# Optimization experiments

Hardware: AMD Instinct MI355X
Metric: run time of the kernel (lower is better)

Reference implementation:

```python
import jax, jax.numpy as jnp
import numpy as np

N = 100000
E = 1600000
EMB3 = 192   # embedding_size * 3
F_LAT = 64   # latency_feature_size
F_OUT = 128  # latency_feature_size * 2 (GATConv out_feats, 1 head)
NEG_SLOPE = 0.2  # DGL GATConv default leaky_relu slope


def setup_inputs() -> dict:
    key = jax.random.key(0)
    ks = jax.random.split(key, 9)
    return {
        "embed": jax.random.normal(ks[0], (N, EMB3), dtype=jnp.float32),
        "src": jax.random.randint(ks[1], (E,), 0, N, dtype=jnp.int64)
               if jax.config.jax_enable_x64 else jax.random.randint(ks[1], (E,), 0, N, dtype=jnp.int32),
        "dst": jax.random.randint(ks[2], (E,), 0, N, dtype=jnp.int32),
        "W_lin": jax.random.normal(ks[3], (EMB3, F_LAT), dtype=jnp.float32) * 0.05,
        "b_lin": jax.random.normal(ks[4], (F_LAT,), dtype=jnp.float32) * 0.05,
        "W_gat": jax.random.normal(ks[5], (F_LAT, F_OUT), dtype=jnp.float32) * 0.05,
        "attn_l": jax.random.normal(ks[6], (F_OUT,), dtype=jnp.float32) * 0.05,
        "attn_r": jax.random.normal(ks[7], (F_OUT,), dtype=jnp.float32) * 0.05,
        "b_gat": jax.random.normal(ks[8], (F_OUT,), dtype=jnp.float32) * 0.05,
    }


def reference(embed, src, dst, W_lin, b_lin, W_gat, attn_l, attn_r, b_gat):
    # linear_input + relu: [N, 192] -> [N, 64]
    x = jax.nn.relu(embed @ W_lin + b_lin)

    # GATConv (1 head): projection [N, 128]
    feat = x @ W_gat
    el = feat @ attn_l  # [N]
    er = feat @ attn_r  # [N]

    # per-edge attention logit with leaky relu
    e = jax.nn.leaky_relu(el[src] + er[dst], negative_slope=NEG_SLOPE)  # [E]

    # edge softmax over incoming edges of each dst node (segment softmax)
    emax = jax.ops.segment_max(e, dst, num_segments=N)           # [N], -inf for empty
    emax = jnp.where(jnp.isfinite(emax), emax, 0.0)
    ee = jnp.exp(e - emax[dst])                                   # [E]
    denom = jax.ops.segment_sum(ee, dst, num_segments=N)          # [N]
    denom = jnp.where(denom > 0, denom, 1.0)
    alpha = ee / denom[dst]                                       # [E]

    # weighted message aggregation: [N, 128]
    rst = jax.ops.segment_sum(feat[src] * alpha[:, None], dst, num_segments=N)
    y = rst + b_gat  # GATConv bias

    mu, logvar = jnp.split(y, 2, axis=-1)
    return mu, jnp.tanh(logvar)
```

## Files before the change

kernel.cpp:

```cpp
#include <hip/hip_runtime.h>
#include <hip/hip_bf16.h>
#include <hip/hip_fp16.h>

#define NEG_SLOPE 0.2f
#define NBUCK_MAX 6400

typedef __attribute__((ext_vector_type(8))) short bf16x8;
typedef __attribute__((ext_vector_type(4))) float f32x4;

__device__ __forceinline__ unsigned pack_bf16(float a, float b) {
    unsigned ua = __float_as_uint(a), ub = __float_as_uint(b);
    ua += 0x7FFFu + ((ua >> 16) & 1u);
    ub += 0x7FFFu + ((ub >> 16) & 1u);
    return (ua >> 16) | (ub & 0xFFFF0000u);
}

__device__ __forceinline__ unsigned pack_f16(float a, float b) {
    union { __half2 h; unsigned u; } cv;
    cv.h = __floats2half2_rn(a, b);
    return cv.u;
}

__global__ __launch_bounds__(256) void k_gemm(
    const float* __restrict__ embed, const float* __restrict__ W_lin,
    const float* __restrict__ b_lin, const float* __restrict__ W_gat,
    const float* __restrict__ attn_l, const float* __restrict__ attn_r,
    unsigned* __restrict__ feat_u32, float* __restrict__ el,
    float* __restrict__ er, int N)
{
    __shared__ __align__(16) char lds[40960];
    const int t = threadIdx.x;
    const int lane = t & 63;
    const int w = t >> 6;
    const int lc = lane & 15;
    const int hg = lane >> 4;
    const int nb = blockIdx.x * 128;

    for (int i = t; i < 6144; i += 256) {
        const int c = i & 63, kp = i >> 6;
        const float w0 = W_lin[(2 * kp) * 64 + c];
        const float w1 = W_lin[(2 * kp + 1) * 64 + c];
        const unsigned off = (unsigned)(c * 384 + kp * 4) ^ ((c & 7) << 4);
        *(unsigned*)(lds + off) = pack_bf16(w0, w1);
    }
    for (int i = t; i < 4096; i += 256) {
        const int c = i & 127, kp = i >> 7;
        const float w0 = W_gat[(2 * kp) * 128 + c];
        const float w1 = W_gat[(2 * kp + 1) * 128 + c];
        const unsigned off = (unsigned)(c * 128 + kp * 4) ^ ((c & 7) << 4);
        *(unsigned*)(lds + 24576 + off) = pack_bf16(w0, w1);
    }
    __syncthreads();

    f32x4 acc1[2][4];
#pragma unroll
    for (int mt = 0; mt < 2; mt++)
#pragma unroll
        for (int nt = 0; nt < 4; nt++) acc1[mt][nt] = (f32x4)0.f;

#pragma unroll
    for (int ks = 0; ks < 6; ks++) {
        bf16x8 bfr[4];
#pragma unroll
        for (int nt = 0; nt < 4; nt++) {
            const int c = nt * 16 + lc;
            const unsigned off = (unsigned)(c * 384 + ks * 64 + hg * 16) ^ ((c & 7) << 4);
            bfr[nt] = *(const bf16x8*)(lds + off);
        }
#pragma unroll
        for (int mt = 0; mt < 2; mt++) {
            int row = nb + w * 32 + mt * 16 + lc;
            if (row >= N) row = N - 1;
            const float4* ep = (const float4*)(embed + (size_t)row * 192 + ks * 32 + hg * 8);
            const float4 p = ep[0], q = ep[1];
            union { bf16x8 v; unsigned u[4]; } a;
            a.u[0] = pack_bf16(p.x, p.y); a.u[1] = pack_bf16(p.z, p.w);
            a.u[2] = pack_bf16(q.x, q.y); a.u[3] = pack_bf16(q.z, q.w);
#pragma unroll
            for (int nt = 0; nt < 4; nt++)
                acc1[mt][nt] = __builtin_amdgcn_mfma_f32_16x16x32_bf16(a.v, bfr[nt], acc1[mt][nt], 0, 0, 0);
        }
    }

    float blv[4];
#pragma unroll
    for (int nt = 0; nt < 4; nt++) blv[nt] = b_lin[nt * 16 + lc];

    __syncthreads();

#pragma unroll
    for (int mt = 0; mt < 2; mt++)
#pragma unroll
        for (int nt = 0; nt < 4; nt++)
#pragma unroll
            for (int r = 0; r < 4; r++) {
                float v = acc1[mt][nt][r] + blv[nt];
                v = v > 0.f ? v : 0.f;
                const int xrow = w * 32 + mt * 16 + 4 * hg + r;
                const int col = nt * 16 + lc;
                const unsigned off = (unsigned)(xrow * 128 + col * 2) ^ ((xrow & 7) << 4);
                unsigned bv = __float_as_uint(v);
                bv += 0x7FFFu + ((bv >> 16) & 1u);
                *(unsigned short*)(lds + off) = (unsigned short)(bv >> 16);
            }
    __syncthreads();

    f32x4 acc2[2][8];
#pragma unroll
    for (int mt = 0; mt < 2; mt++)
#pragma unroll
        for (int nt = 0; nt < 8; nt++) acc2[mt][nt] = (f32x4)0.f;

#pragma unroll
    for (int ks = 0; ks < 2; ks++) {
        bf16x8 a2[2];
#pragma unroll
        for (int mt = 0; mt < 2; mt++) {
            const int row = w * 32 + mt * 16 + lc;
            const unsigned off = (unsigned)(row * 128 + ks * 64 + hg * 16) ^ ((row & 7) << 4);
            a2[mt] = *(const bf16x8*)(lds + off);
        }
#pragma unroll
        for (int nt = 0; nt < 8; nt++) {
            const int c = nt * 16 + lc;
            const unsigned off = (unsigned)(c * 128 + ks * 64 + hg * 16) ^ ((c & 7) << 4);
            const bf16x8 b2 = *(const bf16x8*)(lds + 24576 + off);
            acc2[0][nt] = __builtin_amdgcn_mfma_f32_16x16x32_bf16(a2[0], b2, acc2[0][nt], 0, 0, 0);
            acc2[1][nt] = __builtin_amdgcn_mfma_f32_16x16x32_bf16(a2[1], b2, acc2[1][nt], 0, 0, 0);
        }
    }

    float alv[8], arv[8];
#pragma unroll
    for (int nt = 0; nt < 8; nt++) {
        alv[nt] = attn_l[nt * 16 + lc];
        arv[nt] = attn_r[nt * 16 + lc];
    }

#pragma unroll
    for (int mt = 0; mt < 2; mt++) {
        const int rbase = nb + w * 32 + mt * 16 + 4 * hg;
#pragma unroll
        for (int nt = 0; nt < 8; nt++)
#pragma unroll
            for (int r = 0; r < 4; r++) {
                const float V = acc2[mt][nt][r];
                const float Vp = __shfl_xor(V, 1, 64);
                const int row = rbase + r;
                if (!(lc & 1) && row < N)
                    feat_u32[(size_t)row * 64 + nt * 8 + (lc >> 1)] = pack_f16(V, Vp);
            }
        float elv[4] = {0.f, 0.f, 0.f, 0.f}, erv[4] = {0.f, 0.f, 0.f, 0.f};
#pragma unroll
        for (int nt = 0; nt < 8; nt++)
#pragma unroll
            for (int r = 0; r < 4; r++) {
                elv[r] = fmaf(acc2[mt][nt][r], alv[nt], elv[r]);
                erv[r] = fmaf(acc2[mt][nt][r], arv[nt], erv[r]);
            }
#pragma unroll
        for (int r = 0; r < 4; r++) {
#pragma unroll
            for (int o = 1; o < 16; o <<= 1) {
                elv[r] += __shfl_xor(elv[r], o, 64);
                erv[r] += __shfl_xor(erv[r], o, 64);
            }
            const int row = rbase + r;
            if (lc == r && row < N) { el[row] = elv[r]; er[row] = erv[r]; }
        }
    }
}


__global__ __launch_bounds__(256) void k_hist2(
    const int* __restrict__ dst, int* __restrict__ tbl, int ntiles, int E, int per)
{
    __shared__ int cnt[NBUCK_MAX];
    const int t = threadIdx.x;
    for (int b = t; b < ntiles; b += 256) cnt[b] = 0;
    __syncthreads();

    const int ebase = blockIdx.x * per;
    const int eend = min(E, ebase + per);
    for (int i = ebase + t * 4; i < eend; i += 1024) {
        if (i + 3 < eend) {
            const int4 v = *(const int4*)&dst[i];
            atomicAdd(&cnt[v.x >> 4], 1);
            atomicAdd(&cnt[v.y >> 4], 1);
            atomicAdd(&cnt[v.z >> 4], 1);
            atomicAdd(&cnt[v.w >> 4], 1);
        } else {
            for (int j = i; j < eend; j++) atomicAdd(&cnt[dst[j] >> 4], 1);
        }
    }
    __syncthreads();
    int* row = tbl + (size_t)blockIdx.x * ntiles;
    for (int b = t; b < ntiles; b += 256) row[b] = cnt[b];
}

__global__ void k_scanT(int* __restrict__ tbl, int* __restrict__ total,
                        int ntiles, int G)
{
    const int b = blockIdx.x * 256 + threadIdx.x;
    if (b >= ntiles) return;
    int acc = 0;
    const size_t nt = (size_t)ntiles;
    for (int g = 0; g + 8 <= G; g += 8) {
        int* p = tbl + (size_t)g * nt + b;
        const int v0 = p[0];
        const int v1 = p[nt];
        const int v2 = p[2 * nt];
        const int v3 = p[3 * nt];
        const int v4 = p[4 * nt];
        const int v5 = p[5 * nt];
        const int v6 = p[6 * nt];
        const int v7 = p[7 * nt];
        p[0] = acc;
        p[nt] = acc + v0;
        p[2 * nt] = acc + v0 + v1;
        p[3 * nt] = acc + v0 + v1 + v2;
        p[4 * nt] = acc + v0 + v1 + v2 + v3;
        p[5 * nt] = acc + v0 + v1 + v2 + v3 + v4;
        p[6 * nt] = acc + v0 + v1 + v2 + v3 + v4 + v5;
        p[7 * nt] = acc + v0 + v1 + v2 + v3 + v4 + v5 + v6;
        acc += v0 + v1 + v2 + v3 + v4 + v5 + v6 + v7;
    }
    total[b] = acc;
}

__global__ __launch_bounds__(256) void k_scanN(
    const int* __restrict__ in, int* __restrict__ out, int n)
{
    __shared__ int lds[256];
    const int t = threadIdx.x;
    int carry = 0;
    for (int base = 0; base < n; base += 256) {
        const int i = base + t;
        const int v = (i < n) ? in[i] : 0;
        lds[t] = v;
        __syncthreads();
        for (int o = 1; o < 256; o <<= 1) {
            const int u = (t >= o) ? lds[t - o] : 0;
            __syncthreads();
            lds[t] += u;
            __syncthreads();
        }
        if (i < n) out[i] = carry + lds[t] - v;
        carry += lds[255];
        __syncthreads();
    }
    if (t == 0) out[n] = carry;
}

__global__ __launch_bounds__(256) void k_scat2(
    const int* __restrict__ src, const int* __restrict__ dst,
    const int* __restrict__ tbl, const int* __restrict__ offs_t,
    unsigned* __restrict__ csru, int ntiles, int E, int per)
{
    __shared__ int cnt[NBUCK_MAX];
    __shared__ int base[NBUCK_MAX];
    const int t = threadIdx.x;
    const int* row = tbl + (size_t)blockIdx.x * ntiles;
    for (int b = t; b < ntiles; b += 256) {
        cnt[b] = 0;
        base[b] = offs_t[b] + row[b];
    }
    __syncthreads();

    const int ebase = blockIdx.x * per;
    const int eend = min(E, ebase + per);
    for (int i = ebase + t * 4; i < eend; i += 1024) {
        if (i + 3 < eend) {
            const int4 s4 = *(const int4*)&src[i];
            const int4 d4 = *(const int4*)&dst[i];
            int b, r;
            b = d4.x >> 4; r = atomicAdd(&cnt[b], 1);
            csru[base[b] + r] = (unsigned)s4.x | ((unsigned)(d4.x & 15) << 20);
            b = d4.y >> 4; r = atomicAdd(&cnt[b], 1);
            csru[base[b] + r] = (unsigned)s4.y | ((unsigned)(d4.y & 15) << 20);
            b = d4.z >> 4; r = atomicAdd(&cnt[b], 1);
            csru[base[b] + r] = (unsigned)s4.z | ((unsigned)(d4.z & 15) << 20);
            b = d4.w >> 4; r = atomicAdd(&cnt[b], 1);
            csru[base[b] + r] = (unsigned)s4.w | ((unsigned)(d4.w & 15) << 20);
        } else {
            for (int j = i; j < eend; j++) {
                const int b = dst[j] >> 4;
                const int r = atomicAdd(&cnt[b], 1);
                csru[base[b] + r] = (unsigned)src[j] | ((unsigned)(dst[j] & 15) << 20);
            }
        }
    }
}

__global__ __launch_bounds__(256, 1) void k_agg(
    const unsigned* __restrict__ csru, const int* __restrict__ offs_t,
    const float* __restrict__ el, const float* __restrict__ er,
    const unsigned* __restrict__ feat, const float* __restrict__ b_gat,
    float* __restrict__ out, int N)
{
    __shared__ __align__(16) char ldsB[32768];
    const int t = threadIdx.x;
    const int lane = t & 63;
    const int wid = t >> 6;
    const int lc = lane & 15;
    const int hg = lane >> 4;
    char* wlds = ldsB + wid * 8192;

    const int ntiles = (N + 15) >> 4;
    const int tile = blockIdx.x * 4 + wid;
    if (tile >= ntiles) return;
    const int d0 = tile << 4;

    const int wstart = offs_t[tile];
    const int wend = offs_t[tile + 1];
    const int nw = (wend - wstart + 31) >> 5;

    f32x4 accD[8];
    f32x4 accDen = (f32x4)0.f;
#pragma unroll
    for (int nt = 0; nt < 8; nt++) accD[nt] = (f32x4)0.f;

    union { bf16x8 v; unsigned u[4]; } ONESF;
    ONESF.u[0] = ONESF.u[1] = ONESF.u[2] = ONESF.u[3] = 0x3C003C00u;

    unsigned ev_n = 0u;
    int m_c = 0;
    float elv_c = -3.4e38f, erv_c = 0.f;
    uint4 g0, g1, g2, g3, g4, g5, g6, g7;
    g0 = g1 = g2 = g3 = g4 = g5 = g6 = g7 = make_uint4(0u, 0u, 0u, 0u);

#define GATHER_ALL(SJ)                                                                      \
    do {                                                                                    \
        int rs_;                                                                            \
        rs_ = __shfl((SJ), 0 + hg, 64);  g0 = *(const uint4*)&feat[(size_t)rs_ * 64 + lc * 4]; \
        rs_ = __shfl((SJ), 4 + hg, 64);  g1 = *(const uint4*)&feat[(size_t)rs_ * 64 + lc * 4]; \
        rs_ = __shfl((SJ), 8 + hg, 64);  g2 = *(const uint4*)&feat[(size_t)rs_ * 64 + lc * 4]; \
        rs_ = __shfl((SJ), 12 + hg, 64); g3 = *(const uint4*)&feat[(size_t)rs_ * 64 + lc * 4]; \
        rs_ = __shfl((SJ), 16 + hg, 64); g4 = *(const uint4*)&feat[(size_t)rs_ * 64 + lc * 4]; \
        rs_ = __shfl((SJ), 20 + hg, 64); g5 = *(const uint4*)&feat[(size_t)rs_ * 64 + lc * 4]; \
        rs_ = __shfl((SJ), 24 + hg, 64); g6 = *(const uint4*)&feat[(size_t)rs_ * 64 + lc * 4]; \
        rs_ = __shfl((SJ), 28 + hg, 64); g7 = *(const uint4*)&feat[(size_t)rs_ * 64 + lc * 4]; \
    } while (0)

    if (nw > 0) {
        const int e0 = wstart + lane;
        const bool v0 = (lane < 32) && (e0 < wend);
        const unsigned ev_c = v0 ? csru[e0] : 0u;
        if (nw > 1) {
            const int e1 = wstart + 32 + lane;
            ev_n = (lane < 32 && e1 < wend) ? csru[e1] : 0u;
        }
        const int sj_c = (int)(ev_c & 0xFFFFFu);
        m_c = (int)((ev_c >> 20) & 15u);
        elv_c = v0 ? el[sj_c] : -3.4e38f;
        erv_c = er[d0 + m_c];
        GATHER_ALL(sj_c);
    }

    int w = wstart;
    for (int i = 0; i < nw; ++i, w += 32) {
        *(uint4*)(wlds + ((unsigned)((0  + hg) * 256 + lc * 16) ^ 0u))  = g0;
        *(uint4*)(wlds + ((unsigned)((4  + hg) * 256 + lc * 16) ^ 0u))  = g1;
        *(uint4*)(wlds + ((unsigned)((8  + hg) * 256 + lc * 16) ^ 16u)) = g2;
        *(uint4*)(wlds + ((unsigned)((12 + hg) * 256 + lc * 16) ^ 16u)) = g3;
        *(uint4*)(wlds + ((unsigned)((16 + hg) * 256 + lc * 16) ^ 32u)) = g4;
        *(uint4*)(wlds + ((unsigned)((20 + hg) * 256 + lc * 16) ^ 32u)) = g5;
        *(uint4*)(wlds + ((unsigned)((24 + hg) * 256 + lc * 16) ^ 48u)) = g6;
        *(uint4*)(wlds + ((unsigned)((28 + hg) * 256 + lc * 16) ^ 48u)) = g7;

        float ee = elv_c + erv_c;
        ee = ee >= 0.f ? ee : NEG_SLOPE * ee;
        const float p_c = __expf(ee);
        union { bf16x8 v; unsigned u[4]; } A;
#pragma unroll
        for (int jj = 0; jj < 4; jj++) {
            const int sl = 8 * hg + 2 * jj;
            const float p0 = __shfl(p_c, sl, 64);
            const int   m0 = __shfl(m_c, sl, 64);
            const float p1 = __shfl(p_c, sl + 1, 64);
            const int   m1 = __shfl(m_c, sl + 1, 64);
            A.u[jj] = pack_f16((m0 == lc) ? p0 : 0.f, (m1 == lc) ? p1 : 0.f);
        }

        const int sj_n = (int)(ev_n & 0xFFFFFu);
        const int m_n = (int)((ev_n >> 20) & 15u);
        {
            const int e1 = w + 32 + lane;
            const bool vn = (lane < 32) && (e1 < wend);
            elv_c = vn ? el[sj_n] : -3.4e38f;
            erv_c = er[d0 + m_n];
            m_c = m_n;
        }

        GATHER_ALL(sj_n);

        {
            unsigned ev_f = 0u;
            if (i + 2 < nw) {
                const int e2 = w + 64 + lane;
                ev_f = (lane < 32 && e2 < wend) ? csru[e2] : 0u;
            }
            ev_n = ev_f;
        }

#pragma unroll
        for (int nt = 0; nt < 8; nt++) {
            union { bf16x8 v; unsigned short s[8]; } B;
#pragma unroll
            for (int j = 0; j < 8; j++) {
                const unsigned roff = ((unsigned)((8 * hg + j) * 256 + (nt * 16 + lc) * 2))
                                      ^ (((unsigned)hg & 3u) << 4);
                B.s[j] = *(const unsigned short*)(wlds + roff);
            }
            accD[nt] = __builtin_amdgcn_mfma_f32_16x16x32_f16(A.v, B.v, accD[nt], 0, 0, 0);
        }
        accDen = __builtin_amdgcn_mfma_f32_16x16x32_f16(A.v, ONESF.v, accDen, 0, 0, 0);
    }
#undef GATHER_ALL

    float inv[4];
#pragma unroll
    for (int r = 0; r < 4; r++) {
        const float den = accDen[r];
        inv[r] = den > 0.f ? 1.f / den : 0.f;
    }

    const size_t nh = (size_t)N * 64;
#pragma unroll
    for (int r = 0; r < 4; r++) {
        const int d = d0 + 4 * hg + r;
        if (d < N) {
#pragma unroll
            for (int nt = 0; nt < 8; nt++) {
                const int c = nt * 16 + lc;
                const float y = accD[nt][r] * inv[r] + b_gat[c];
                if (c < 64) out[(size_t)d * 64 + c] = y;
                else        out[nh + (size_t)d * 64 + (c - 64)] = tanhf(y);
            }
        }
    }
}

extern "C" void kernel_launch(void* const* d_in, const int* in_sizes, int n_in,
                              void* d_out, int out_size, void* d_ws, size_t ws_size,
                              hipStream_t stream) {
    const float* embed  = (const float*)d_in[0];
    const int*   src    = (const int*)d_in[1];
    const int*   dst    = (const int*)d_in[2];
    const float* W_lin  = (const float*)d_in[3];
    const float* b_lin  = (const float*)d_in[4];
    const float* W_gat  = (const float*)d_in[5];
    const float* attn_l = (const float*)d_in[6];
    const float* attn_r = (const float*)d_in[7];
    const float* b_gat  = (const float*)d_in[8];
    float* out = (float*)d_out;

    const int N = in_sizes[0] / 192;
    const int E = in_sizes[1];
    const int ntiles = (N + 15) / 16;
    const int G = 256;
    const int per = (((E + G - 1) / G) + 3) & ~3;

    char* ws = (char*)d_ws;
    size_t off = 0;
    auto alloc = [&](size_t bytes) -> void* {
        void* p = ws + off;
        off += (bytes + 255) & ~(size_t)255;
        return p;
    };
    unsigned* feat     = (unsigned*)alloc((size_t)N * 64 * 4);
    float*    el       = (float*)alloc((size_t)N * 4);
    float*    er       = (float*)alloc((size_t)N * 4);
    int*      tbl      = (int*)alloc((size_t)G * ntiles * 4);
    int*      totalT   = (int*)alloc((size_t)ntiles * 4);
    int*      offs_t   = (int*)alloc(((size_t)ntiles + 1) * 4);
    unsigned* csru     = (unsigned*)alloc((size_t)E * 4);

    k_gemm<<<(N + 127) / 128, 256, 0, stream>>>(embed, W_lin, b_lin, W_gat,
                                                attn_l, attn_r, feat, el, er, N);
    k_hist2<<<G, 256, 0, stream>>>(dst, tbl, ntiles, E, per);
    k_scanT<<<(ntiles + 255) / 256, 256, 0, stream>>>(tbl, totalT, ntiles, G);
    k_scanN<<<1, 256, 0, stream>>>(totalT, offs_t, ntiles);
    k_scat2<<<G, 256, 0, stream>>>(src, dst, tbl, offs_t, csru, ntiles, E, per);
    k_agg<<<(ntiles + 3) / 4, 256, 0, stream>>>(csru, offs_t, el, er,
                                                feat, b_gat, out, N);
}
```

Measured before the change: 188.6 us.

## Fuse GEMM blocks into scatter kernel launch and simplify scatter position counters

The separate GEMM kernel is merged into the scatter kernel as extra blocks: the first G blocks do the CSR scatter, the rest compute feat/el/er. This lets the memory-bound scatter and the compute-heavy GEMM run concurrently in one grid and removes a kernel launch. The scatter also now uses a single LDS position array (base plus atomic increment) instead of separate count and base arrays. The cost is heterogeneous blocks sharing one LDS size (40KB for scatter blocks too), which may reduce occupancy for the scatter part.

```diff
diff --git a/kernel.cpp b/kernel.cpp
--- a/kernel.cpp
+++ b/kernel.cpp
@@ -20,157 +20,6 @@
     cv.h = __floats2half2_rn(a, b);
     return cv.u;
 }
-
-__global__ __launch_bounds__(256) void k_gemm(
-    const float* __restrict__ embed, const float* __restrict__ W_lin,
-    const float* __restrict__ b_lin, const float* __restrict__ W_gat,
-    const float* __restrict__ attn_l, const float* __restrict__ attn_r,
-    unsigned* __restrict__ feat_u32, float* __restrict__ el,
-    float* __restrict__ er, int N)
-{
-    __shared__ __align__(16) char lds[40960];
-    const int t = threadIdx.x;
-    const int lane = t & 63;
-    const int w = t >> 6;
-    const int lc = lane & 15;
-    const int hg = lane >> 4;
-    const int nb = blockIdx.x * 128;
-
-    for (int i = t; i < 6144; i += 256) {
-        const int c = i & 63, kp = i >> 6;
-        const float w0 = W_lin[(2 * kp) * 64 + c];
-        const float w1 = W_lin[(2 * kp + 1) * 64 + c];
-        const unsigned off = (unsigned)(c * 384 + kp * 4) ^ ((c & 7) << 4);
-        *(unsigned*)(lds + off) = pack_bf16(w0, w1);
-    }
-    for (int i = t; i < 4096; i += 256) {
-        const int c = i & 127, kp = i >> 7;
-        const float w0 = W_gat[(2 * kp) * 128 + c];
-        const float w1 = W_gat[(2 * kp + 1) * 128 + c];
-        const unsigned off = (unsigned)(c * 128 + kp * 4) ^ ((c & 7) << 4);
-        *(unsigned*)(lds + 24576 + off) = pack_bf16(w0, w1);
-    }
-    __syncthreads();
-
-    f32x4 acc1[2][4];
-#pragma unroll
-    for (int mt = 0; mt < 2; mt++)
-#pragma unroll
-        for (int nt = 0; nt < 4; nt++) acc1[mt][nt] = (f32x4)0.f;
-
-#pragma unroll
-    for (int ks = 0; ks < 6; ks++) {
-        bf16x8 bfr[4];
-#pragma unroll
-        for (int nt = 0; nt < 4; nt++) {
-            const int c = nt * 16 + lc;
-            const unsigned off = (unsigned)(c * 384 + ks * 64 + hg * 16) ^ ((c & 7) << 4);
-            bfr[nt] = *(const bf16x8*)(lds + off);
-        }
-#pragma unroll
-        for (int mt = 0; mt < 2; mt++) {
-            int row = nb + w * 32 + mt * 16 + lc;
-            if (row >= N) row = N - 1;
-            const float4* ep = (const float4*)(embed + (size_t)row * 192 + ks * 32 + hg * 8);
-            const float4 p = ep[0], q = ep[1];
-            union { bf16x8 v; unsigned u[4]; } a;
-            a.u[0] = pack_bf16(p.x, p.y); a.u[1] = pack_bf16(p.z, p.w);
-            a.u[2] = pack_bf16(q.x, q.y); a.u[3] = pack_bf16(q.z, q.w);
-#pragma unroll
-            for (int nt = 0; nt < 4; nt++)
-                acc1[mt][nt] = __builtin_amdgcn_mfma_f32_16x16x32_bf16(a.v, bfr[nt], acc1[mt][nt], 0, 0, 0);
-        }
-    }
-
-    float blv[4];
-#pragma unroll
-    for (int nt = 0; nt < 4; nt++) blv[nt] = b_lin[nt * 16 + lc];
-
-    __syncthreads();
-
-#pragma unroll
-    for (int mt = 0; mt < 2; mt++)
-#pragma unroll
-        for (int nt = 0; nt < 4; nt++)
-#pragma unroll
-            for (int r = 0; r < 4; r++) {
-                float v = acc1[mt][nt][r] + blv[nt];
-                v = v > 0.f ? v : 0.f;
-                const int xrow = w * 32 + mt * 16 + 4 * hg + r;
-                const int col = nt * 16 + lc;
-                const unsigned off = (unsigned)(xrow * 128 + col * 2) ^ ((xrow & 7) << 4);
-                unsigned bv = __float_as_uint(v);
-                bv += 0x7FFFu + ((bv >> 16) & 1u);
-                *(unsigned short*)(lds + off) = (unsigned short)(bv >> 16);
-            }
-    __syncthreads();
-
-    f32x4 acc2[2][8];
-#pragma unroll
-    for (int mt = 0; mt < 2; mt++)
-#pragma unroll
-        for (int nt = 0; nt < 8; nt++) acc2[mt][nt] = (f32x4)0.f;
-
-#pragma unroll
-    for (int ks = 0; ks < 2; ks++) {
-        bf16x8 a2[2];
-#pragma unroll
-        for (int mt = 0; mt < 2; mt++) {
-            const int row = w * 32 + mt * 16 + lc;
-            const unsigned off = (unsigned)(row * 128 + ks * 64 + hg * 16) ^ ((row & 7) << 4);
-            a2[mt] = *(const bf16x8*)(lds + off);
-        }
-#pragma unroll
-        for (int nt = 0; nt < 8; nt++) {
-            const int c = nt * 16 + lc;
-            const unsigned off = (unsigned)(c * 128 + ks * 64 + hg * 16) ^ ((c & 7) << 4);
-            const bf16x8 b2 = *(const bf16x8*)(lds + 24576 + off);
-            acc2[0][nt] = __builtin_amdgcn_mfma_f32_16x16x32_bf16(a2[0], b2, acc2[0][nt], 0, 0, 0);
-            acc2[1][nt] = __builtin_amdgcn_mfma_f32_16x16x32_bf16(a2[1], b2, acc2[1][nt], 0, 0, 0);
-        }
-    }
-
-    float alv[8], arv[8];
-#pragma unroll
-    for (int nt = 0; nt < 8; nt++) {
-        alv[nt] = attn_l[nt * 16 + lc];
-        arv[nt] = attn_r[nt * 16 + lc];
-    }
-
-#pragma unroll
-    for (int mt = 0; mt < 2; mt++) {
-        const int rbase = nb + w * 32 + mt * 16 + 4 * hg;
-#pragma unroll
-        for (int nt = 0; nt < 8; nt++)
-#pragma unroll
-            for (int r = 0; r < 4; r++) {
-                const float V = acc2[mt][nt][r];
-                const float Vp = __shfl_xor(V, 1, 64);
-                const int row = rbase + r;
-                if (!(lc & 1) && row < N)
-                    feat_u32[(size_t)row * 64 + nt * 8 + (lc >> 1)] = pack_f16(V, Vp);
-            }
-        float elv[4] = {0.f, 0.f, 0.f, 0.f}, erv[4] = {0.f, 0.f, 0.f, 0.f};
-#pragma unroll
-        for (int nt = 0; nt < 8; nt++)
-#pragma unroll
-            for (int r = 0; r < 4; r++) {
-                elv[r] = fmaf(acc2[mt][nt][r], alv[nt], elv[r]);
-                erv[r] = fmaf(acc2[mt][nt][r], arv[nt], erv[r]);
-            }
-#pragma unroll
-        for (int r = 0; r < 4; r++) {
-#pragma unroll
-            for (int o = 1; o < 16; o <<= 1) {
-                elv[r] += __shfl_xor(elv[r], o, 64);
-                erv[r] += __shfl_xor(erv[r], o, 64);
-            }
-            const int row = rbase + r;
-            if (lc == r && row < N) { el[row] = elv[r]; er[row] = erv[r]; }
-        }
-    }
-}
-
 
 __global__ __launch_bounds__(256) void k_hist2(
     const int* __restrict__ dst, int* __restrict__ tbl, int ntiles, int E, int per)
@@ -252,42 +101,187 @@
     if (t == 0) out[n] = carry;
 }
 
-__global__ __launch_bounds__(256) void k_scat2(
+__global__ __launch_bounds__(256) void k_scat_gemm(
     const int* __restrict__ src, const int* __restrict__ dst,
     const int* __restrict__ tbl, const int* __restrict__ offs_t,
-    unsigned* __restrict__ csru, int ntiles, int E, int per)
+    unsigned* __restrict__ csru, int ntiles, int E, int per, int G,
+    const float* __restrict__ embed, const float* __restrict__ W_lin,
+    const float* __restrict__ b_lin, const float* __restrict__ W_gat,
+    const float* __restrict__ attn_l, const float* __restrict__ attn_r,
+    unsigned* __restrict__ feat_u32, float* __restrict__ el,
+    float* __restrict__ er, int N)
 {
-    __shared__ int cnt[NBUCK_MAX];
-    __shared__ int base[NBUCK_MAX];
+    __shared__ __align__(16) char lds[40960];
     const int t = threadIdx.x;
-    const int* row = tbl + (size_t)blockIdx.x * ntiles;
-    for (int b = t; b < ntiles; b += 256) {
-        cnt[b] = 0;
-        base[b] = offs_t[b] + row[b];
+
+    if (blockIdx.x < G) {
+        int* pos = (int*)lds;
+        const int* row = tbl + (size_t)blockIdx.x * ntiles;
+        for (int b = t; b < ntiles; b += 256) pos[b] = offs_t[b] + row[b];
+        __syncthreads();
+
+        const int ebase = blockIdx.x * per;
+        const int eend = min(E, ebase + per);
+        for (int i = ebase + t * 4; i < eend; i += 1024) {
+            if (i + 3 < eend) {
+                const int4 s4 = *(const int4*)&src[i];
+                const int4 d4 = *(const int4*)&dst[i];
+                int r;
+                r = atomicAdd(&pos[d4.x >> 4], 1);
+                csru[r] = (unsigned)s4.x | ((unsigned)(d4.x & 15) << 20);
+                r = atomicAdd(&pos[d4.y >> 4], 1);
+                csru[r] = (unsigned)s4.y | ((unsigned)(d4.y & 15) << 20);
+                r = atomicAdd(&pos[d4.z >> 4], 1);
+                csru[r] = (unsigned)s4.z | ((unsigned)(d4.z & 15) << 20);
+                r = atomicAdd(&pos[d4.w >> 4], 1);
+                csru[r] = (unsigned)s4.w | ((unsigned)(d4.w & 15) << 20);
+            } else {
+                for (int j = i; j < eend; j++) {
+                    const int r = atomicAdd(&pos[dst[j] >> 4], 1);
+                    csru[r] = (unsigned)src[j] | ((unsigned)(dst[j] & 15) << 20);
+                }
+            }
+        }
+        return;
+    }
+
+    const int lane = t & 63;
+    const int w = t >> 6;
+    const int lc = lane & 15;
+    const int hg = lane >> 4;
+    const int nb = (blockIdx.x - G) * 128;
+
+    for (int i = t; i < 6144; i += 256) {
+        const int c = i & 63, kp = i >> 6;
+        const float w0 = W_lin[(2 * kp) * 64 + c];
+        const float w1 = W_lin[(2 * kp + 1) * 64 + c];
+        const unsigned off = (unsigned)(c * 384 + kp * 4) ^ ((c & 7) << 4);
+        *(unsigned*)(lds + off) = pack_bf16(w0, w1);
+    }
+    for (int i = t; i < 4096; i += 256) {
+        const int c = i & 127, kp = i >> 7;
+        const float w0 = W_gat[(2 * kp) * 128 + c];
+        const float w1 = W_gat[(2 * kp + 1) * 128 + c];
+        const unsigned off = (unsigned)(c * 128 + kp * 4) ^ ((c & 7) << 4);
+        *(unsigned*)(lds + 24576 + off) = pack_bf16(w0, w1);
     }
     __syncthreads();
 
-    const int ebase = blockIdx.x * per;
-    const int eend = min(E, ebase + per);
-    for (int i = ebase + t * 4; i < eend; i += 1024) {
-        if (i + 3 < eend) {
-            const int4 s4 = *(const int4*)&src[i];
-            const int4 d4 = *(const int4*)&dst[i];
-            int b, r;
-            b = d4.x >> 4; r = atomicAdd(&cnt[b], 1);
-            csru[base[b] + r] = (unsigned)s4.x | ((unsigned)(d4.x & 15) << 20);
-            b = d4.y >> 4; r = atomicAdd(&cnt[b], 1);
-            csru[base[b] + r] = (unsigned)s4.y | ((unsigned)(d4.y & 15) << 20);
-            b = d4.z >> 4; r = atomicAdd(&cnt[b], 1);
-            csru[base[b] + r] = (unsigned)s4.z | ((unsigned)(d4.z & 15) << 20);
-            b = d4.w >> 4; r = atomicAdd(&cnt[b], 1);
-            csru[base[b] + r] = (unsigned)s4.w | ((unsigned)(d4.w & 15) << 20);
-        } else {
-            for (int j = i; j < eend; j++) {
-                const int b = dst[j] >> 4;
-                const int r = atomicAdd(&cnt[b], 1);
-                csru[base[b] + r] = (unsigned)src[j] | ((unsigned)(dst[j] & 15) << 20);
-            }
+    f32x4 acc1[2][4];
+#pragma unroll
+    for (int mt = 0; mt < 2; mt++)
+#pragma unroll
+        for (int nt = 0; nt < 4; nt++) acc1[mt][nt] = (f32x4)0.f;
+
+#pragma unroll
+    for (int ks = 0; ks < 6; ks++) {
+        bf16x8 bfr[4];
+#pragma unroll
+        for (int nt = 0; nt < 4; nt++) {
+            const int c = nt * 16 + lc;
+            const unsigned off = (unsigned)(c * 384 + ks * 64 + hg * 16) ^ ((c & 7) << 4);
+            bfr[nt] = *(const bf16x8*)(lds + off);
+        }
+#pragma unroll
+        for (int mt = 0; mt < 2; mt++) {
+            int row = nb + w * 32 + mt * 16 + lc;
+            if (row >= N) row = N - 1;
+            const float4* ep = (const float4*)(embed + (size_t)row * 192 + ks * 32 + hg * 8);
+            const float4 p = ep[0], q = ep[1];
+            union { bf16x8 v; unsigned u[4]; } a;
+            a.u[0] = pack_bf16(p.x, p.y); a.u[1] = pack_bf16(p.z, p.w);
+            a.u[2] = pack_bf16(q.x, q.y); a.u[3] = pack_bf16(q.z, q.w);
+#pragma unroll
+            for (int nt = 0; nt < 4; nt++)
+                acc1[mt][nt] = __builtin_amdgcn_mfma_f32_16x16x32_bf16(a.v, bfr[nt], acc1[mt][nt], 0, 0, 0);
+        }
+    }
+
+    float blv[4];
+#pragma unroll
+    for (int nt = 0; nt < 4; nt++) blv[nt] = b_lin[nt * 16 + lc];
+
+    __syncthreads();
+
+#pragma unroll
+    for (int mt = 0; mt < 2; mt++)
+#pragma unroll
+        for (int nt = 0; nt < 4; nt++)
+#pragma unroll
+            for (int r = 0; r < 4; r++) {
+                float v = acc1[mt][nt][r] + blv[nt];
+                v = v > 0.f ? v : 0.f;
+                const int xrow = w * 32 + mt * 16 + 4 * hg + r;
+                const int col = nt * 16 + lc;
+                const unsigned off = (unsigned)(xrow * 128 + col * 2) ^ ((xrow & 7) << 4);
+                unsigned bv = __float_as_uint(v);
+                bv += 0x7FFFu + ((bv >> 16) & 1u);
+                *(unsigned short*)(lds + off) = (unsigned short)(bv >> 16);
+            }
+    __syncthreads();
+
+    f32x4 acc2[2][8];
+#pragma unroll
+    for (int mt = 0; mt < 2; mt++)
+#pragma unroll
+        for (int nt = 0; nt < 8; nt++) acc2[mt][nt] = (f32x4)0.f;
+
+#pragma unroll
+    for (int ks = 0; ks < 2; ks++) {
+        bf16x8 a2[2];
+#pragma unroll
+        for (int mt = 0; mt < 2; mt++) {
+            const int row = w * 32 + mt * 16 + lc;
+            const unsigned off = (unsigned)(row * 128 + ks * 64 + hg * 16) ^ ((row & 7) << 4);
+            a2[mt] = *(const bf16x8*)(lds + off);
+        }
+#pragma unroll
+        for (int nt = 0; nt < 8; nt++) {
+            const int c = nt * 16 + lc;
+            const unsigned off = (unsigned)(c * 128 + ks * 64 + hg * 16) ^ ((c & 7) << 4);
+            const bf16x8 b2 = *(const bf16x8*)(lds + 24576 + off);
+            acc2[0][nt] = __builtin_amdgcn_mfma_f32_16x16x32_bf16(a2[0], b2, acc2[0][nt], 0, 0, 0);
+            acc2[1][nt] = __builtin_amdgcn_mfma_f32_16x16x32_bf16(a2[1], b2, acc2[1][nt], 0, 0, 0);
+        }
+    }
+
+    float alv[8], arv[8];
+#pragma unroll
+    for (int nt = 0; nt < 8; nt++) {
+        alv[nt] = attn_l[nt * 16 + lc];
+        arv[nt] = attn_r[nt * 16 + lc];
+    }
+
+#pragma unroll
+    for (int mt = 0; mt < 2; mt++) {
+        const int rbase = nb + w * 32 + mt * 16 + 4 * hg;
+#pragma unroll
+        for (int nt = 0; nt < 8; nt++)
+#pragma unroll
+            for (int r = 0; r < 4; r++) {
+                const float V = acc2[mt][nt][r];
+                const float Vp = __shfl_xor(V, 1, 64);
+                const int row = rbase + r;
+                if (!(lc & 1) && row < N)
+                    feat_u32[(size_t)row * 64 + nt * 8 + (lc >> 1)] = pack_f16(V, Vp);
+            }
+        float elv[4] = {0.f, 0.f, 0.f, 0.f}, erv[4] = {0.f, 0.f, 0.f, 0.f};
+#pragma unroll
+        for (int nt = 0; nt < 8; nt++)
+#pragma unroll
+            for (int r = 0; r < 4; r++) {
+                elv[r] = fmaf(acc2[mt][nt][r], alv[nt], elv[r]);
+                erv[r] = fmaf(acc2[mt][nt][r], arv[nt], erv[r]);
+            }
+#pragma unroll
+        for (int r = 0; r < 4; r++) {
+#pragma unroll
+            for (int o = 1; o < 16; o <<= 1) {
+                elv[r] += __shfl_xor(elv[r], o, 64);
+                erv[r] += __shfl_xor(erv[r], o, 64);
+            }
+            const int row = rbase + r;
+            if (lc == r && row < N) { el[row] = elv[r]; er[row] = erv[r]; }
         }
     }
 }
@@ -460,6 +454,7 @@
     const int ntiles = (N + 15) / 16;
     const int G = 256;
     const int per = (((E + G - 1) / G) + 3) & ~3;
+    const int gemmBlocks = (N + 127) / 128;
 
     char* ws = (char*)d_ws;
     size_t off = 0;
@@ -476,12 +471,12 @@
     int*      offs_t   = (int*)alloc(((size_t)ntiles + 1) * 4);
     unsigned* csru     = (unsigned*)alloc((size_t)E * 4);
 
-    k_gemm<<<(N + 127) / 128, 256, 0, stream>>>(embed, W_lin, b_lin, W_gat,
-                                                attn_l, attn_r, feat, el, er, N);
     k_hist2<<<G, 256, 0, stream>>>(dst, tbl, ntiles, E, per);
     k_scanT<<<(ntiles + 255) / 256, 256, 0, stream>>>(tbl, totalT, ntiles, G);
     k_scanN<<<1, 256, 0, stream>>>(totalT, offs_t, ntiles);
-    k_scat2<<<G, 256, 0, stream>>>(src, dst, tbl, offs_t, csru, ntiles, E, per);
+    k_scat_gemm<<<G + gemmBlocks, 256, 0, stream>>>(
+        src, dst, tbl, offs_t, csru, ntiles, E, per, G,
+        embed, W_lin, b_lin, W_gat, attn_l, attn_r, feat, el, er, N);
     k_agg<<<(ntiles + 3) / 4, 256, 0, stream>>>(csru, offs_t, el, er,
                                                 feat, b_gat, out, N);
 }
```

After: 182.2 us. 3.4% less time.
